# Kernel tuning notes

Measured on AMD Instinct MI355X. Metric: run time of the kernel, lower is better.

The kernel has to match this reference:

```python
import jax, jax.numpy as jnp
import numpy as np

SMOOTH = 1.0
ALPHA = 0.7
BETA = 0.3
GAMMA = 4.0 / 3.0


def setup_inputs() -> dict:
    key = jax.random.key(0)
    k1, k2 = jax.random.split(key)
    inputs = jax.random.normal(k1, (8, 10, 512, 512), dtype=jnp.float32)
    targets = jax.random.randint(k2, (8, 512, 512), 0, 10, dtype=jnp.int32)
    return {"inputs": inputs, "targets": targets}


def reference(inputs, targets):
    # inputs: [B, C, H, W] logits; targets: [B, H, W] int labels, 0 = ignore.
    C = inputs.shape[1]
    # ignore_index=0: drop the background channel before softmax/argmax
    logits = inputs[:, 1:]                      # [B, C-1, H, W]
    probs = jax.nn.softmax(logits, axis=1)
    # argmax over remaining channels -> map back to original labels 1..C-1
    preds = jnp.argmax(probs, axis=1).astype(jnp.int32) + 1   # [B, H, W]

    t = targets.reshape(-1)
    p = preds.reshape(-1)
    mask = t != 0                               # drop ignore-class pixels

    # per-class confusion counts via fused histograms (classes 1..C-1)
    tp = jnp.bincount(jnp.where(mask & (p == t), t, 0), length=C)[1:]
    tgt_cnt = jnp.bincount(jnp.where(mask, t, 0), length=C)[1:]
    pred_cnt = jnp.bincount(jnp.where(mask, p, 0), length=C)[1:]

    TP = tp.astype(jnp.float32)
    FN = (tgt_cnt - tp).astype(jnp.float32)
    FP = (pred_cnt - tp).astype(jnp.float32)

    tversky = (TP + SMOOTH) / (TP + ALPHA * FN + BETA * FP + SMOOTH)
    return jnp.sum((1.0 - tversky) ** GAMMA)
```

## Files before the change

kernel.cpp:

```cpp
#include <hip/hip_runtime.h>


#define HW4     65536
#define NGROUPS 524288
#define NBLK    2048

__global__ __launch_bounds__(256) void ftl_hist(const float* __restrict__ inp,
                                                const int* __restrict__ tgt,
                                                unsigned int* __restrict__ pw) {
    __shared__ unsigned int s[4][27];
    const int tid  = threadIdx.x;
    const int wave = tid >> 6;
    const int lane = tid & 63;

    const int i  = blockIdx.x * 256 + tid;
    const int b  = i >> 16;
    const int gi = i & (HW4 - 1);

    const float4* base = reinterpret_cast<const float4*>(inp)
                       + (((size_t)(b * 10 + 1)) << 16) + gi;

    float4 v = base[0];
    float bv0 = v.x, bv1 = v.y, bv2 = v.z, bv3 = v.w;
    int   bc0 = 1,   bc1 = 1,   bc2 = 1,   bc3 = 1;
#pragma unroll
    for (int c = 2; c <= 9; ++c) {
        float4 w = base[((size_t)(c - 1)) << 16];
        if (w.x > bv0) { bv0 = w.x; bc0 = c; }
        if (w.y > bv1) { bv1 = w.y; bc1 = c; }
        if (w.z > bv2) { bv2 = w.z; bc2 = c; }
        if (w.w > bv3) { bv3 = w.w; bc3 = c; }
    }

    const int4 t = reinterpret_cast<const int4*>(tgt)[i];

    unsigned int cTP[9], cT[9], cP[9];
#pragma unroll
    for (int j = 0; j < 9; ++j) { cTP[j] = 0u; cT[j] = 0u; cP[j] = 0u; }

    const unsigned long long vx = __ballot(t.x != 0);
    const unsigned long long vy = __ballot(t.y != 0);
    const unsigned long long vz = __ballot(t.z != 0);
    const unsigned long long vw = __ballot(t.w != 0);

#pragma unroll
    for (int c = 1; c <= 9; ++c) {
        const int j = c - 1;
        {
            const unsigned long long tm = __ballot(t.x == c);
            const unsigned long long pm = __ballot(bc0 == c);
            cT[j]  += (unsigned int)__builtin_popcountll(tm);
            cP[j]  += (unsigned int)__builtin_popcountll(pm & vx);
            cTP[j] += (unsigned int)__builtin_popcountll(tm & pm);
        }
        {
            const unsigned long long tm = __ballot(t.y == c);
            const unsigned long long pm = __ballot(bc1 == c);
            cT[j]  += (unsigned int)__builtin_popcountll(tm);
            cP[j]  += (unsigned int)__builtin_popcountll(pm & vy);
            cTP[j] += (unsigned int)__builtin_popcountll(tm & pm);
        }
        {
            const unsigned long long tm = __ballot(t.z == c);
            const unsigned long long pm = __ballot(bc2 == c);
            cT[j]  += (unsigned int)__builtin_popcountll(tm);
            cP[j]  += (unsigned int)__builtin_popcountll(pm & vz);
            cTP[j] += (unsigned int)__builtin_popcountll(tm & pm);
        }
        {
            const unsigned long long tm = __ballot(t.w == c);
            const unsigned long long pm = __ballot(bc3 == c);
            cT[j]  += (unsigned int)__builtin_popcountll(tm);
            cP[j]  += (unsigned int)__builtin_popcountll(pm & vw);
            cTP[j] += (unsigned int)__builtin_popcountll(tm & pm);
        }
    }

    if (lane == 0) {
#pragma unroll
        for (int j = 0; j < 9; ++j) {
            s[wave][j]      = cTP[j];
            s[wave][9 + j]  = cT[j];
            s[wave][18 + j] = cP[j];
        }
    }
    __syncthreads();
    if (tid < 27)
        pw[tid * NBLK + blockIdx.x] = s[0][tid] + s[1][tid] + s[2][tid] + s[3][tid];
}

__global__ __launch_bounds__(896) void ftl_reduce(const unsigned int* __restrict__ pw,
                                                  float* __restrict__ out) {
    __shared__ double cs[27];
    const int tid = threadIdx.x;
    const int g = tid >> 5;
    const int l = tid & 31;
    if (g < 27) {
        unsigned int sum = 0;
        const unsigned int* row = pw + g * NBLK;
#pragma unroll 8
        for (int k = l; k < NBLK; k += 32) sum += row[k];
#pragma unroll
        for (int off = 16; off; off >>= 1) sum += __shfl_down(sum, off, 32);
        if (l == 0) cs[g] = (double)sum;
    }
    __syncthreads();
    if (tid == 0) {
        double loss = 0.0;
#pragma unroll
        for (int c = 0; c < 9; ++c) {
            const double TP = cs[c];
            const double FN = cs[9 + c]  - TP;
            const double FP = cs[18 + c] - TP;
            const double tv = (TP + 1.0) / (TP + 0.7 * FN + 0.3 * FP + 1.0);
            loss += pow(1.0 - tv, 4.0 / 3.0);
        }
        out[0] = (float)loss;
    }
}

extern "C" void kernel_launch(void* const* d_in, const int* in_sizes, int n_in,
                              void* d_out, int out_size, void* d_ws, size_t ws_size,
                              hipStream_t stream) {
    const float* inp = (const float*)d_in[0];
    const int*   tgt = (const int*)d_in[1];
    unsigned int* pw = (unsigned int*)d_ws;
    float* out = (float*)d_out;

    ftl_hist<<<dim3(NBLK), dim3(256), 0, stream>>>(inp, tgt, pw);
    ftl_reduce<<<dim3(1), dim3(896), 0, stream>>>(pw, out);
}
```

Before: 132.0 us.

## Fuse final reduction into histogram kernel via atomics and last-block finalize

Drops the separate single-block reduce kernel. Each block atomically adds its 27 counts into a global accumulator, and the last block to finish, detected with an atomic ticket counter, computes the loss. This removes one kernel launch and the partials round trip, but adds a memset launch and contended atomics on 27 addresses from 2048 blocks.

```diff
diff --git a/kernel.cpp b/kernel.cpp
--- a/kernel.cpp
+++ b/kernel.cpp
@@ -5,9 +5,10 @@
 #define NGROUPS 524288
 #define NBLK    2048
 
-__global__ __launch_bounds__(256) void ftl_hist(const float* __restrict__ inp,
-                                                const int* __restrict__ tgt,
-                                                unsigned int* __restrict__ pw) {
+__global__ __launch_bounds__(256) void ftl_fused(const float* __restrict__ inp,
+                                                 const int* __restrict__ tgt,
+                                                 unsigned int* __restrict__ acc,
+                                                 float* __restrict__ out) {
     __shared__ unsigned int s[4][27];
     const int tid  = threadIdx.x;
     const int wave = tid >> 6;
@@ -85,25 +86,21 @@
         }
     }
     __syncthreads();
+
     if (tid < 27)
-        pw[tid * NBLK + blockIdx.x] = s[0][tid] + s[1][tid] + s[2][tid] + s[3][tid];
-}
+        atomicAdd(&acc[tid], s[0][tid] + s[1][tid] + s[2][tid] + s[3][tid]);
 
-__global__ __launch_bounds__(896) void ftl_reduce(const unsigned int* __restrict__ pw,
-                                                  float* __restrict__ out) {
+    __threadfence();
+    __syncthreads();
+    __shared__ unsigned int lastFlag;
+    if (tid == 0)
+        lastFlag = (atomicAdd(&acc[27], 1u) == NBLK - 1) ? 1u : 0u;
+    __syncthreads();
+    if (!lastFlag) return;
+
     __shared__ double cs[27];
-    const int tid = threadIdx.x;
-    const int g = tid >> 5;
-    const int l = tid & 31;
-    if (g < 27) {
-        unsigned int sum = 0;
-        const unsigned int* row = pw + g * NBLK;
-#pragma unroll 8
-        for (int k = l; k < NBLK; k += 32) sum += row[k];
-#pragma unroll
-        for (int off = 16; off; off >>= 1) sum += __shfl_down(sum, off, 32);
-        if (l == 0) cs[g] = (double)sum;
-    }
+    if (tid < 27)
+        cs[tid] = (double)atomicAdd(&acc[tid], 0u);
     __syncthreads();
     if (tid == 0) {
         double loss = 0.0;
@@ -124,9 +121,9 @@
                               hipStream_t stream) {
     const float* inp = (const float*)d_in[0];
     const int*   tgt = (const int*)d_in[1];
-    unsigned int* pw = (unsigned int*)d_ws;
+    unsigned int* acc = (unsigned int*)d_ws;
     float* out = (float*)d_out;
 
-    ftl_hist<<<dim3(NBLK), dim3(256), 0, stream>>>(inp, tgt, pw);
-    ftl_reduce<<<dim3(1), dim3(896), 0, stream>>>(pw, out);
+    hipMemsetAsync(acc, 0, 32 * sizeof(unsigned int), stream);
+    ftl_fused<<<dim3(NBLK), dim3(256), 0, stream>>>(inp, tgt, acc, out);
 }
```

Measured after the change: 411.6 us. 212% more time.
